# Performance work log

Measured on AMD Instinct MI355X. Metric: run time of the kernel, lower is better.

The kernel has to match this reference:

```python
import jax, jax.numpy as jnp
import numpy as np

N, E, G = 50000, 1600000, 512
H, NF_IN, NF_OUT, GF_OUT, EDIM, DEPTH = 128, 64, 64, 128, 16, 3
EPS = 1e-5


def seg_softmax(logits, seg, num):
    m = jax.ops.segment_max(logits, seg, num_segments=num)
    e = jnp.exp(logits - m[seg])
    s = jax.ops.segment_sum(e, seg, num_segments=num)
    return e / s[seg]


def batchnorm_train(x, gamma, beta):
    mu = jnp.mean(x, axis=0)
    var = jnp.mean((x - mu) ** 2, axis=0)  # biased, as torch BN training
    return (x - mu) * jax.lax.rsqrt(var + EPS) * gamma + beta


def setup_inputs() -> dict:
    key = jax.random.key(0)
    ks = jax.random.split(key, 20)
    inp = {}
    inp['x'] = jax.random.normal(ks[0], (N, NF_IN), jnp.float32)
    inp['edge_index'] = jax.random.randint(ks[1], (2, E), 0, N, jnp.int64)
    inp['edge_attr'] = jax.random.normal(ks[2], (E, EDIM), jnp.float32)
    inp['batch'] = jnp.sort(jax.random.randint(ks[3], (N,), 0, G, jnp.int64))
    inp['num_graphs'] = G
    s = 0.05
    inp['Wi'] = jax.random.normal(ks[4], (H, NF_IN), jnp.float32) * s
    inp['bi'] = jnp.zeros((H,), jnp.float32)
    inp['gat_W'] = jax.random.normal(ks[5], (DEPTH, H, 2 * H), jnp.float32) * s
    inp['gat_a'] = jax.random.normal(ks[6], (DEPTH, 2 * H), jnp.float32) * s
    inp['nfW1'] = jax.random.normal(ks[7], (H, H), jnp.float32) * s
    inp['nfb1'] = jnp.zeros((H,), jnp.float32)
    inp['nf_g'] = jnp.ones((H,), jnp.float32)
    inp['nf_b'] = jnp.zeros((H,), jnp.float32)
    inp['nfW2'] = jax.random.normal(ks[8], (NF_OUT, H), jnp.float32) * s
    inp['nfb2'] = jnp.zeros((NF_OUT,), jnp.float32)
    inp['gfW1'] = jax.random.normal(ks[9], (H, H), jnp.float32) * s
    inp['gfb1'] = jnp.zeros((H,), jnp.float32)
    inp['gf_g'] = jnp.ones((H,), jnp.float32)
    inp['gf_b'] = jnp.zeros((H,), jnp.float32)
    inp['gfW2'] = jax.random.normal(ks[10], (GF_OUT, H), jnp.float32) * s
    inp['gfb2'] = jnp.zeros((GF_OUT,), jnp.float32)
    return inp


def reference(x, edge_index, edge_attr, batch, num_graphs, Wi, bi, gat_W, gat_a,
              nfW1, nfb1, nf_g, nf_b, nfW2, nfb2,
              gfW1, gfb1, gf_g, gf_b, gfW2, gfb2):
    src, dst = edge_index[0], edge_index[1]
    nf = x @ Wi.T + bi  # [N,H]
    for i in range(DEPTH):
        src_nf = nf[src]            # [E,H]
        dst_nf = nf[dst]            # [E,H]
        ef = jnp.concatenate([src_nf, dst_nf], axis=-1) @ gat_a[i]  # [E]
        alpha = seg_softmax(ef, dst, N)
        agg = jax.ops.segment_sum(alpha[:, None] * src_nf, dst, num_segments=N)
        nf = jax.nn.relu(jnp.concatenate([nf, agg], axis=-1) @ gat_W[i].T)
    # 3-iteration attention pooling over graphs
    h = nf
    for _ in range(3):
        logits = jnp.sum(h * nf, axis=-1)  # [N]
        alpha = seg_softmax(logits, batch, num_graphs)
        h = alpha[:, None] * nf
    gf = jax.ops.segment_sum(h, batch, num_segments=num_graphs)  # [G,H]
    nf_out = jax.nn.relu(batchnorm_train(nf @ nfW1.T + nfb1, nf_g, nf_b)) @ nfW2.T + nfb2
    gf_out = jax.nn.relu(batchnorm_train(gf @ gfW1.T + gfb1, gf_g, gf_b)) @ gfW2.T + gfb2
    return nf_out, edge_attr, gf_out
```

## Files before the change

### kernel.cpp

```cpp
#include <hip/hip_runtime.h>

#define NN 50000
#define NE 1600000
#define NG 512
#define HD 128
#define NGRP 8
#define GRPSZ ((NN + NGRP - 1) / NGRP)
#define PCAP 28672

typedef __attribute__((ext_vector_type(8))) short bf16x8;
typedef __attribute__((ext_vector_type(4))) float f32x4;

static __device__ __forceinline__ unsigned bf16rn(float x) {
  unsigned b = __float_as_uint(x);
  return (b + 0x7FFFu + ((b >> 16) & 1u)) >> 16;
}
static __device__ __forceinline__ float bf16tof(unsigned short u) {
  return __uint_as_float(((unsigned)u) << 16);
}

__global__ void __launch_bounds__(256) k_part(const int* __restrict__ src,
                                              const int* __restrict__ dst,
                                              uint2* __restrict__ pairs,
                                              int* __restrict__ pcnt) {
  __shared__ uint2 buf[8][512];
  __shared__ int lcnt[8];
  __shared__ int gbase[8];
  __shared__ int nfl[8];
  const int tid = threadIdx.x;
  const int b = blockIdx.x & 7;
  if (tid < 8) lcnt[tid] = 0;
  __syncthreads();
  const int stride = gridDim.x * 256;
  for (int base_e = blockIdx.x * 256; base_e < NE; base_e += stride) {
    int e = base_e + tid;
    bool valid = e < NE;
    if (valid) {
      int d = dst[e];
      int s = src[e];
      int g = d / GRPSZ;
      int pos = atomicAdd(&lcnt[g], 1);
      buf[g][pos] = make_uint2((unsigned)d, (unsigned)s);
    }
    __syncthreads();
    if (tid < 8) {
      int c = lcnt[tid];
      int nf = (c >= 256) ? 256 : 0;
      nfl[tid] = nf;
      gbase[tid] = nf ? atomicAdd(&pcnt[tid * 8 + b], nf) : 0;
    }
    __syncthreads();
#pragma unroll
    for (int g0 = 0; g0 < 8; ++g0) {
      if (nfl[g0]) {
        int gb = gbase[g0] + tid;
        if (gb < PCAP)
          pairs[(size_t)(g0 * 8 + b) * PCAP + gb] = buf[g0][tid];
      }
    }
    __syncthreads();
#pragma unroll
    for (int g0 = 0; g0 < 8; ++g0) {
      if (nfl[g0]) {
        int rem = lcnt[g0] - 256;
        if (tid < rem) buf[g0][tid] = buf[g0][256 + tid];
      }
    }
    __syncthreads();
    if (tid < 8 && nfl[tid]) lcnt[tid] -= 256;
    __syncthreads();
  }
  if (tid < 8) {
    int c = lcnt[tid];
    gbase[tid] = c ? atomicAdd(&pcnt[tid * 8 + b], c) : 0;
  }
  __syncthreads();
#pragma unroll
  for (int g0 = 0; g0 < 8; ++g0) {
    int c = lcnt[g0];
    if (tid < c) {
      int gb = gbase[g0] + tid;
      if (gb < PCAP)
        pairs[(size_t)(g0 * 8 + b) * PCAP + gb] = buf[g0][tid];
    }
  }
}

__global__ void __launch_bounds__(256) k_hist(const uint2* __restrict__ pairs,
                                              const int* __restrict__ pcnt,
                                              int* __restrict__ hcnt) {
  __shared__ int hist[GRPSZ];
  const int b = blockIdx.x;
  const int g = b & 7, sub = b >> 3;
  const int li = g * 8 + sub;
  const int lo = g * GRPSZ;
  for (int i = threadIdx.x; i < GRPSZ; i += 256) hist[i] = 0;
  __syncthreads();
  int cnt = min(pcnt[li], PCAP);
  const uint2* lst = pairs + (size_t)li * PCAP;
  for (int i = threadIdx.x; i < cnt; i += 256)
    atomicAdd(&hist[(int)lst[i].x - lo], 1);
  __syncthreads();
  for (int i = threadIdx.x; i < GRPSZ; i += 256)
    hcnt[(size_t)li * GRPSZ + i] = hist[i];
}

__global__ void __launch_bounds__(256) k_csr(const uint2* __restrict__ pairs,
                                             const int* __restrict__ pcnt,
                                             const int* __restrict__ hcnt,
                                             int* __restrict__ row_ptr,
                                             int* __restrict__ csr_src) {
  __shared__ int rp[GRPSZ];
  __shared__ int cur[GRPSZ];
  __shared__ int wsum[256];
  const int b = blockIdx.x;
  const int g = b & 7, sub = b >> 3;
  const int li = g * 8 + sub;
  const int lo = g * GRPSZ;
  int gbase = 0;
  for (int gg = 0; gg < g; ++gg)
#pragma unroll
    for (int ss = 0; ss < 8; ++ss) gbase += pcnt[gg * 8 + ss];
  for (int i = threadIdx.x; i < GRPSZ; i += 256) {
    int dsum = 0, before = 0;
#pragma unroll
    for (int ss = 0; ss < 8; ++ss) {
      int h = hcnt[(size_t)(g * 8 + ss) * GRPSZ + i];
      dsum += h;
      if (ss < sub) before += h;
    }
    rp[i] = dsum;
    cur[i] = before;
  }
  __syncthreads();
  const int CH = (GRPSZ + 255) / 256;
  int t0 = threadIdx.x * CH;
  int t1 = min(GRPSZ, t0 + CH);
  int s = 0;
  for (int i = t0; i < t1; ++i) { int v = rp[i]; rp[i] = s; s += v; }
  wsum[threadIdx.x] = s;
  __syncthreads();
  for (int off = 1; off < 256; off <<= 1) {
    int t = ((int)threadIdx.x >= off) ? wsum[threadIdx.x - off] : 0;
    __syncthreads();
    wsum[threadIdx.x] += t;
    __syncthreads();
  }
  int add = gbase + ((threadIdx.x > 0) ? wsum[threadIdx.x - 1] : 0);
  for (int i = t0; i < t1; ++i) rp[i] += add;
  __syncthreads();
  for (int i = threadIdx.x; i < GRPSZ; i += 256) {
    cur[i] += rp[i];
    if (sub == 0) row_ptr[lo + i] = rp[i];
  }
  if (sub == 0 && g == 7 && threadIdx.x == 0) row_ptr[NN] = NE;
  __syncthreads();
  int cnt = min(pcnt[li], PCAP);
  const uint2* lst = pairs + (size_t)li * PCAP;
  for (int i = threadIdx.x; i < cnt; i += 256) {
    uint2 p = lst[i];
    int pos = atomicAdd(&cur[(int)p.x - lo], 1);
    csr_src[pos] = (int)p.y;
  }
}

__global__ void k_init_bounds(int* __restrict__ gs, int* __restrict__ ge) {
  int g = blockIdx.x * 256 + threadIdx.x;
  if (g < NG) { gs[g] = NN; ge[g] = 0; }
}
__global__ void k_bounds(const int* __restrict__ batch, int* __restrict__ gs, int* __restrict__ ge) {
  int n = blockIdx.x * 256 + threadIdx.x;
  if (n < NN) {
    int b = batch[n];
    atomicMin(&gs[b], n);
    atomicMax(&ge[b], n + 1);
  }
}

__global__ void k_cvt3(const float* __restrict__ a0, int n0,
                       const float* __restrict__ a1, int n1,
                       const float* __restrict__ a2, int n2,
                       unsigned short* __restrict__ b) {
  int i = blockIdx.x * 256 + threadIdx.x;
  if (i >= n0 + n1 + n2) return;
  float v = (i < n0) ? a0[i] : (i < n0 + n1) ? a1[i - n0] : a2[i - n0 - n1];
  b[i] = (unsigned short)bf16rn(v);
}

__global__ void k_gat_agg(const uint4* __restrict__ nf16u4, const float* __restrict__ e1,
                          const int* __restrict__ row_ptr, const int* __restrict__ csr_src,
                          unsigned short* __restrict__ agg16) {
  int node = blockIdx.x * 4 + (threadIdx.x >> 6);
  int lane = threadIdx.x & 63;
  if (node >= NN) return;
  int s = row_ptr[node], e = row_ptr[node + 1];
  const int q = lane >> 3;
  const int c = lane & 7;

  float acc[16];
#pragma unroll
  for (int i = 0; i < 16; ++i) acc[i] = 0.f;
  float zloc = 0.f;

  int jj = s + q;
  bool v0 = jj < e;
  int sc = v0 ? csr_src[jj] : 0;
  float w = v0 ? e1[sc] : 0.f;
  uint4 u0 = nf16u4[(size_t)sc * 16 + c * 2];
  uint4 u1 = nf16u4[(size_t)sc * 16 + c * 2 + 1];

  for (int j = s; j < e; j += 8) {
    int jn = j + 8 + q;
    bool vn = jn < e;
    int scn = vn ? csr_src[jn] : 0;
    float wn = vn ? e1[scn] : 0.f;
    uint4 un0 = nf16u4[(size_t)scn * 16 + c * 2];
    uint4 un1 = nf16u4[(size_t)scn * 16 + c * 2 + 1];
    zloc += w;
    acc[0]  = fmaf(w, __uint_as_float(u0.x << 16), acc[0]);
    acc[1]  = fmaf(w, __uint_as_float(u0.x & 0xFFFF0000u), acc[1]);
    acc[2]  = fmaf(w, __uint_as_float(u0.y << 16), acc[2]);
    acc[3]  = fmaf(w, __uint_as_float(u0.y & 0xFFFF0000u), acc[3]);
    acc[4]  = fmaf(w, __uint_as_float(u0.z << 16), acc[4]);
    acc[5]  = fmaf(w, __uint_as_float(u0.z & 0xFFFF0000u), acc[5]);
    acc[6]  = fmaf(w, __uint_as_float(u0.w << 16), acc[6]);
    acc[7]  = fmaf(w, __uint_as_float(u0.w & 0xFFFF0000u), acc[7]);
    acc[8]  = fmaf(w, __uint_as_float(u1.x << 16), acc[8]);
    acc[9]  = fmaf(w, __uint_as_float(u1.x & 0xFFFF0000u), acc[9]);
    acc[10] = fmaf(w, __uint_as_float(u1.y << 16), acc[10]);
    acc[11] = fmaf(w, __uint_as_float(u1.y & 0xFFFF0000u), acc[11]);
    acc[12] = fmaf(w, __uint_as_float(u1.z << 16), acc[12]);
    acc[13] = fmaf(w, __uint_as_float(u1.z & 0xFFFF0000u), acc[13]);
    acc[14] = fmaf(w, __uint_as_float(u1.w << 16), acc[14]);
    acc[15] = fmaf(w, __uint_as_float(u1.w & 0xFFFF0000u), acc[15]);
    sc = scn; w = wn; u0 = un0; u1 = un1;
  }

  zloc += __shfl_xor(zloc, 8);
  zloc += __shfl_xor(zloc, 16);
  zloc += __shfl_xor(zloc, 32);
  float inv = (zloc > 0.f) ? 1.f / zloc : 0.f;
#pragma unroll
  for (int i = 0; i < 16; ++i) {
    acc[i] += __shfl_xor(acc[i], 8);
    acc[i] += __shfl_xor(acc[i], 16);
    acc[i] += __shfl_xor(acc[i], 32);
    acc[i] *= inv;
  }
  if (q == 0) {
    uint4 p0, p1;
    p0.x = bf16rn(acc[0])  | (bf16rn(acc[1])  << 16);
    p0.y = bf16rn(acc[2])  | (bf16rn(acc[3])  << 16);
    p0.z = bf16rn(acc[4])  | (bf16rn(acc[5])  << 16);
    p0.w = bf16rn(acc[6])  | (bf16rn(acc[7])  << 16);
    p1.x = bf16rn(acc[8])  | (bf16rn(acc[9])  << 16);
    p1.y = bf16rn(acc[10]) | (bf16rn(acc[11]) << 16);
    p1.z = bf16rn(acc[12]) | (bf16rn(acc[13]) << 16);
    p1.w = bf16rn(acc[14]) | (bf16rn(acc[15]) << 16);
    uint4* dst = (uint4*)(agg16 + (size_t)node * HD + c * 16);
    dst[0] = p0;
    dst[1] = p1;
  }
}

template <int K, int KA, int HO, bool RELUOUT, bool BIAS, bool OUTF32, bool OUT16, int DOTM>
__global__ void __launch_bounds__(256) k_mfma(
    const unsigned short* __restrict__ A1, const unsigned short* __restrict__ A2,
    const unsigned short* __restrict__ W16, const float* __restrict__ bias,
    float* __restrict__ outf, unsigned short* __restrict__ out16,
    const float* __restrict__ dvec, float* __restrict__ dout, int nrows) {
  constexpr int NT = HO / 16;
  const int l = threadIdx.x & 63;
  const int w = threadIdx.x >> 6;
  const int lr = l & 15;
  const int q = l >> 4;
  const int row0 = blockIdx.x * 64 + w * 16;
  const int arow = min(row0 + lr, nrows - 1);
  const unsigned short* pa1 = A1 + (size_t)arow * KA;
  const unsigned short* pa2 = (KA < K) ? (A2 + (size_t)arow * (K - KA)) : nullptr;

  f32x4 acc[NT];
#pragma unroll
  for (int t = 0; t < NT; ++t) acc[t] = (f32x4){0.f, 0.f, 0.f, 0.f};

#pragma unroll
  for (int s = 0; s < K / 32; ++s) {
    const int kg = s * 32 + q * 8;
    bf16x8 af;
    if constexpr (KA == K) {
      af = *(const bf16x8*)(pa1 + kg);
    } else {
      af = (s * 32 < KA) ? *(const bf16x8*)(pa1 + kg)
                         : *(const bf16x8*)(pa2 + (kg - KA));
    }
#pragma unroll
    for (int t = 0; t < NT; ++t) {
      bf16x8 bfr = *(const bf16x8*)(W16 + (size_t)(t * 16 + lr) * K + kg);
      acc[t] = __builtin_amdgcn_mfma_f32_16x16x32_bf16(af, bfr, acc[t], 0, 0, 0);
    }
  }

  float bv[BIAS ? NT : 1];
  if constexpr (BIAS) {
#pragma unroll
    for (int t = 0; t < NT; ++t) bv[t] = bias[t * 16 + lr];
  }
  float dv[DOTM == 1 ? NT : 1];
  if constexpr (DOTM == 1) {
#pragma unroll
    for (int t = 0; t < NT; ++t) dv[t] = dvec[t * 16 + lr];
  }
  float p[4] = {0.f, 0.f, 0.f, 0.f};
#pragma unroll
  for (int j = 0; j < 4; ++j) {
    int n = row0 + q * 4 + j;
    bool ok = n < nrows;
#pragma unroll
    for (int t = 0; t < NT; ++t) {
      float v = acc[t][j];
      if constexpr (BIAS) v += bv[t];
      if constexpr (RELUOUT) v = fmaxf(v, 0.f);
      if (ok) {
        if constexpr (OUTF32) outf[(size_t)n * HO + t * 16 + lr] = v;
        if constexpr (OUT16) out16[(size_t)n * HO + t * 16 + lr] = (unsigned short)bf16rn(v);
      }
      if constexpr (DOTM == 1) p[j] = fmaf(v, dv[t], p[j]);
      if constexpr (DOTM == 2) p[j] = fmaf(v, v, p[j]);
    }
  }
  if constexpr (DOTM != 0) {
#pragma unroll
    for (int j = 0; j < 4; ++j) {
      p[j] += __shfl_xor(p[j], 1);
      p[j] += __shfl_xor(p[j], 2);
      p[j] += __shfl_xor(p[j], 4);
      p[j] += __shfl_xor(p[j], 8);
    }
    if (lr == 0) {
#pragma unroll
      for (int j = 0; j < 4; ++j) {
        int n = row0 + q * 4 + j;
        if (n < nrows) dout[n] = (DOTM == 1) ? __expf(p[j]) : p[j];
      }
    }
  }
}

template <int K, int KA, int HO, bool PRE, bool RELUOUT, bool BIAS, bool OUT16, int DOTM>
__global__ void __launch_bounds__(256) k_gemm(
    const float* __restrict__ inA, const float* __restrict__ inB,
    const float* __restrict__ W, const float* __restrict__ bias,
    const float* __restrict__ preA, const float* __restrict__ preB,
    float* __restrict__ out, int nrows,
    unsigned* __restrict__ out16, const float* __restrict__ dvec,
    float* __restrict__ dout) {
  constexpr int KC = 64;
  constexpr int BM = 64;
  constexpr int MT = 4;
  constexpr int NT = HO / 16;
  constexpr int LDW = HO + 4;
  constexpr int LDA = KC + 4;

  __shared__ float Wl[KC * LDW];
  __shared__ float inl[BM * LDA];

  const int tid = threadIdx.x;
  const int tr = tid >> 4;
  const int tc = tid & 15;
  const int row0 = blockIdx.x * BM;
  const int r0 = tr * MT;
  const int c0 = tc * NT;

  float acc[MT][NT];
#pragma unroll
  for (int i = 0; i < MT; ++i)
#pragma unroll
    for (int j = 0; j < NT; ++j) acc[i][j] = BIAS ? bias[c0 + j] : 0.f;

  for (int cc = 0; cc < K / KC; ++cc) {
    const int k0 = cc * KC;
    if (cc) __syncthreads();
    for (int idx = tid; idx < HO * (KC / 4); idx += 256) {
      int h = idx >> 4;
      int qq = idx & 15;
      float4 w = *(const float4*)(W + (size_t)h * K + k0 + qq * 4);
      Wl[(qq * 4 + 0) * LDW + h] = w.x;
      Wl[(qq * 4 + 1) * LDW + h] = w.y;
      Wl[(qq * 4 + 2) * LDW + h] = w.z;
      Wl[(qq * 4 + 3) * LDW + h] = w.w;
    }
    for (int idx = tid; idx < BM * (KC / 4); idx += 256) {
      int r = idx >> 4;
      int qq = idx & 15;
      int n = row0 + r;
      int kg = k0 + qq * 4;
      float4 v = make_float4(0.f, 0.f, 0.f, 0.f);
      if (n < nrows) {
        if constexpr (KA == K) {
          v = *(const float4*)(inA + (size_t)n * K + kg);
        } else {
          if (k0 < KA) v = *(const float4*)(inA + (size_t)n * KA + kg);
          else         v = *(const float4*)(inB + (size_t)n * (K - KA) + kg - KA);
        }
      }
      if constexpr (PRE) {
        v.x = fmaxf(v.x * preA[kg + 0] + preB[kg + 0], 0.f);
        v.y = fmaxf(v.y * preA[kg + 1] + preB[kg + 1], 0.f);
        v.z = fmaxf(v.z * preA[kg + 2] + preB[kg + 2], 0.f);
        v.w = fmaxf(v.w * preA[kg + 3] + preB[kg + 3], 0.f);
      }
      *(float4*)(inl + r * LDA + qq * 4) = v;
    }
    __syncthreads();
#pragma unroll 8
    for (int k = 0; k < KC; ++k) {
      float a[MT];
#pragma unroll
      for (int i = 0; i < MT; ++i) a[i] = inl[(r0 + i) * LDA + k];
      float4 b0 = *(const float4*)(Wl + k * LDW + c0);
#pragma unroll
      for (int i = 0; i < MT; ++i) {
        acc[i][0] = fmaf(a[i], b0.x, acc[i][0]);
        acc[i][1] = fmaf(a[i], b0.y, acc[i][1]);
        acc[i][2] = fmaf(a[i], b0.z, acc[i][2]);
        acc[i][3] = fmaf(a[i], b0.w, acc[i][3]);
      }
      if constexpr (NT == 8) {
        float4 b1 = *(const float4*)(Wl + k * LDW + c0 + 4);
#pragma unroll
        for (int i = 0; i < MT; ++i) {
          acc[i][4] = fmaf(a[i], b1.x, acc[i][4]);
          acc[i][5] = fmaf(a[i], b1.y, acc[i][5]);
          acc[i][6] = fmaf(a[i], b1.z, acc[i][6]);
          acc[i][7] = fmaf(a[i], b1.w, acc[i][7]);
        }
      }
    }
  }
  float dv[DOTM == 1 ? NT : 1];
  if constexpr (DOTM == 1) {
#pragma unroll
    for (int j = 0; j < NT; ++j) dv[j] = dvec[c0 + j];
  }
#pragma unroll
  for (int i = 0; i < MT; ++i) {
    int n = row0 + r0 + i;
    if constexpr (RELUOUT) {
#pragma unroll
      for (int j = 0; j < NT; ++j) acc[i][j] = fmaxf(acc[i][j], 0.f);
    }
    if (n < nrows) {
      float4 o0 = make_float4(acc[i][0], acc[i][1], acc[i][2], acc[i][3]);
      *(float4*)(out + (size_t)n * HO + c0) = o0;
      if constexpr (NT == 8) {
        float4 o1 = make_float4(acc[i][4], acc[i][5], acc[i][6], acc[i][7]);
        *(float4*)(out + (size_t)n * HO + c0 + 4) = o1;
      }
      if constexpr (OUT16 && NT == 8) {
        uint4 pk;
        pk.x = bf16rn(acc[i][0]) | (bf16rn(acc[i][1]) << 16);
        pk.y = bf16rn(acc[i][2]) | (bf16rn(acc[i][3]) << 16);
        pk.z = bf16rn(acc[i][4]) | (bf16rn(acc[i][5]) << 16);
        pk.w = bf16rn(acc[i][6]) | (bf16rn(acc[i][7]) << 16);
        *(uint4*)(out16 + (size_t)n * 64 + tc * 4) = pk;
      }
    }
    if constexpr (DOTM != 0) {
      float p = 0.f;
#pragma unroll
      for (int j = 0; j < NT; ++j)
        p = fmaf(acc[i][j], (DOTM == 1) ? dv[j] : acc[i][j], p);
      p += __shfl_xor(p, 1);
      p += __shfl_xor(p, 2);
      p += __shfl_xor(p, 4);
      p += __shfl_xor(p, 8);
      if (tc == 0 && n < nrows) dout[n] = (DOTM == 1) ? __expf(p) : p;
    }
  }
}

__global__ void k_pool(const unsigned short* __restrict__ nf16, const float* __restrict__ r,
                       const int* __restrict__ gs, const int* __restrict__ ge,
                       float* __restrict__ alpha, float* __restrict__ gf) {
  int g = blockIdx.x;
  int s = gs[g], e = ge[g];
  __shared__ float red[256];
  for (int it = 0; it < 3; ++it) {
    float lm = -INFINITY;
    for (int n = s + threadIdx.x; n < e; n += 256) {
      float l = r[n];
      if (it) l *= alpha[n];
      lm = fmaxf(lm, l);
    }
    red[threadIdx.x] = lm;
    __syncthreads();
    for (int off = 128; off > 0; off >>= 1) {
      if ((int)threadIdx.x < off) red[threadIdx.x] = fmaxf(red[threadIdx.x], red[threadIdx.x + off]);
      __syncthreads();
    }
    float m = red[0];
    __syncthreads();
    float zz = 0.f;
    for (int n = s + threadIdx.x; n < e; n += 256) {
      float l = r[n];
      if (it) l *= alpha[n];
      zz += __expf(l - m);
    }
    red[threadIdx.x] = zz;
    __syncthreads();
    for (int off = 128; off > 0; off >>= 1) {
      if ((int)threadIdx.x < off) red[threadIdx.x] += red[threadIdx.x + off];
      __syncthreads();
    }
    float z = red[0];
    __syncthreads();
    float invz = 1.f / z;
    for (int n = s + threadIdx.x; n < e; n += 256) {
      float l = r[n];
      if (it) l *= alpha[n];
      alpha[n] = __expf(l - m) * invz;
    }
    __syncthreads();
  }
  int c = threadIdx.x & 127;
  int rr2 = threadIdx.x >> 7;
  float acc = 0.f;
  for (int n = s + rr2; n < e; n += 2)
    acc += alpha[n] * bf16tof(nf16[(size_t)n * HD + c]);
  red[threadIdx.x] = acc;
  __syncthreads();
  if (rr2 == 0) gf[(size_t)g * HD + c] = red[threadIdx.x] + red[threadIdx.x + 128];
}

__global__ void k_colstats(const float* __restrict__ y, float* __restrict__ sum,
                           float* __restrict__ sumsq, int R, int CH) {
  int c = threadIdx.x & 127;
  int rr = threadIdx.x >> 7;
  int r0 = blockIdx.x * CH;
  int r1 = min(R, r0 + CH);
  float s = 0.f, q = 0.f;
  for (int r = r0 + rr; r < r1; r += 2) {
    float v = y[(size_t)r * HD + c];
    s += v;
    q += v * v;
  }
  __shared__ float ls[256], lq[256];
  ls[threadIdx.x] = s;
  lq[threadIdx.x] = q;
  __syncthreads();
  if (rr == 0) {
    s += ls[threadIdx.x + 128];
    q += lq[threadIdx.x + 128];
    atomicAdd(&sum[c], s);
    atomicAdd(&sumsq[c], q);
  }
}

__global__ void k_bn_final(const float* __restrict__ sum, const float* __restrict__ sumsq,
                           const float* __restrict__ g, const float* __restrict__ b,
                           float* __restrict__ A, float* __restrict__ B, float R) {
  int c = threadIdx.x;
  float mu = sum[c] / R;
  float var = sumsq[c] / R - mu * mu;
  float a = g[c] * rsqrtf(var + 1e-5f);
  A[c] = a;
  B[c] = b[c] - mu * a;
}

__global__ void k_bnapply(const float* __restrict__ y, const float* __restrict__ Ac,
                          const float* __restrict__ Bc, unsigned short* __restrict__ z) {
  int i = blockIdx.x * 256 + threadIdx.x;
  if (i >= NN * 16) return;
  int c = (i & 15) * 8;
  const float4* yp = (const float4*)y + (size_t)i * 2;
  float4 v0 = yp[0], v1 = yp[1];
  float4 a0 = *(const float4*)(Ac + c), a1 = *(const float4*)(Ac + c + 4);
  float4 b0 = *(const float4*)(Bc + c), b1 = *(const float4*)(Bc + c + 4);
  float r0 = fmaxf(fmaf(v0.x, a0.x, b0.x), 0.f);
  float r1 = fmaxf(fmaf(v0.y, a0.y, b0.y), 0.f);
  float r2 = fmaxf(fmaf(v0.z, a0.z, b0.z), 0.f);
  float r3 = fmaxf(fmaf(v0.w, a0.w, b0.w), 0.f);
  float r4 = fmaxf(fmaf(v1.x, a1.x, b1.x), 0.f);
  float r5 = fmaxf(fmaf(v1.y, a1.y, b1.y), 0.f);
  float r6 = fmaxf(fmaf(v1.z, a1.z, b1.z), 0.f);
  float r7 = fmaxf(fmaf(v1.w, a1.w, b1.w), 0.f);
  uint4 pk;
  pk.x = bf16rn(r0) | (bf16rn(r1) << 16);
  pk.y = bf16rn(r2) | (bf16rn(r3) << 16);
  pk.z = bf16rn(r4) | (bf16rn(r5) << 16);
  pk.w = bf16rn(r6) | (bf16rn(r7) << 16);
  *(uint4*)(z + (size_t)i * 8) = pk;
}

__global__ void k_copy4(const float4* __restrict__ a, float4* __restrict__ b, int n) {
  int i = blockIdx.x * 256 + threadIdx.x;
  if (i < n) b[i] = a[i];
}

extern "C" void kernel_launch(void* const* d_in, const int* in_sizes, int n_in,
                              void* d_out, int out_size, void* d_ws, size_t ws_size,
                              hipStream_t stream) {
  const float* x        = (const float*)d_in[0];
  const int*   ei       = (const int*)d_in[1];
  const float* edge_attr= (const float*)d_in[2];
  const int*   batch    = (const int*)d_in[3];
  const float* Wi       = (const float*)d_in[5];
  const float* bi       = (const float*)d_in[6];
  const float* gat_W    = (const float*)d_in[7];
  const float* gat_a    = (const float*)d_in[8];
  const float* nfW1     = (const float*)d_in[9];
  const float* nfb1     = (const float*)d_in[10];
  const float* nf_g     = (const float*)d_in[11];
  const float* nf_b     = (const float*)d_in[12];
  const float* nfW2     = (const float*)d_in[13];
  const float* nfb2     = (const float*)d_in[14];
  const float* gfW1     = (const float*)d_in[15];
  const float* gfb1     = (const float*)d_in[16];
  const float* gf_g     = (const float*)d_in[17];
  const float* gf_b     = (const float*)d_in[18];
  const float* gfW2     = (const float*)d_in[19];
  const float* gfb2     = (const float*)d_in[20];

  float* out = (float*)d_out;

  unsigned short* nf16A = (unsigned short*)d_ws;
  unsigned short* nf16B = nf16A + (size_t)NN * HD;
  unsigned short* agg16 = nf16B + (size_t)NN * HD;
  unsigned short* z16   = agg16 + (size_t)NN * HD;
  unsigned short* wt_gat = z16 + (size_t)NN * HD;
  unsigned short* wt_nf1 = wt_gat + 3 * 128 * 256;
  unsigned short* wt_nf2 = wt_nf1 + 128 * 128;
  float* nfA   = (float*)(wt_nf2 + 64 * 128);
  float* e1v   = nfA + (size_t)NN * HD;
  float* rv    = e1v + NN;
  float* alpha = rv + NN;
  float* gf    = alpha + NN;
  float* gy    = gf + (size_t)NG * HD;
  int*   pcnt  = (int*)(gy + (size_t)NG * HD);
  float* sums  = (float*)(pcnt + 64);
  float* sums2 = sums + 256;
  float* bnAB  = sums2 + 256;
  int* row_ptr = (int*)(bnAB + 256);
  int* csr_src = row_ptr + NN + 1;
  int* gs      = csr_src + NE;
  int* ge      = gs + NG;
  int* hcnt    = ge + NG;
  uint2* pairs = (uint2*)nfA;

  const int* src  = ei;
  const int* dstp = ei + NE;

  hipMemsetAsync(pcnt, 0, (64 + 512) * sizeof(int), stream);

  k_part<<<512, 256, 0, stream>>>(src, dstp, pairs, pcnt);
  k_hist<<<64, 256, 0, stream>>>(pairs, pcnt, hcnt);
  k_csr<<<64, 256, 0, stream>>>(pairs, pcnt, hcnt, row_ptr, csr_src);

  k_init_bounds<<<2, 256, 0, stream>>>(gs, ge);
  k_bounds<<<(NN + 255) / 256, 256, 0, stream>>>(batch, gs, ge);

  k_cvt3<<<(3 * 128 * 256 + 128 * 128 + 64 * 128 + 255) / 256, 256, 0, stream>>>(
      gat_W, 3 * 128 * 256, nfW1, 128 * 128, nfW2, 64 * 128, wt_gat);

  k_gemm<64, 64, 128, false, false, true, true, 1><<<(NN + 63) / 64, 256, 0, stream>>>(
      x, nullptr, Wi, bi, nullptr, nullptr, nfA, NN, (unsigned*)nf16A, gat_a, e1v);

  unsigned short* cur = nf16A;
  unsigned short* nxt = nf16B;
  const int gemm_grid = (NN + 63) / 64;
  for (int l = 0; l < 3; ++l) {
    k_gat_agg<<<(NN + 3) / 4, 256, 0, stream>>>((const uint4*)cur, e1v, row_ptr, csr_src, agg16);
    if (l < 2) {
      k_mfma<256, 128, 128, true, false, false, true, 1><<<gemm_grid, 256, 0, stream>>>(
          cur, agg16, wt_gat + (size_t)l * 128 * 256, nullptr,
          nullptr, nxt, gat_a + (size_t)(l + 1) * 256, e1v, NN);
    } else {
      k_mfma<256, 128, 128, true, false, false, true, 2><<<gemm_grid, 256, 0, stream>>>(
          cur, agg16, wt_gat + (size_t)l * 128 * 256, nullptr,
          nullptr, nxt, nullptr, rv, NN);
    }
    unsigned short* t = cur; cur = nxt; nxt = t;
  }

  k_pool<<<NG, 256, 0, stream>>>(cur, rv, gs, ge, alpha, gf);

  k_mfma<128, 128, 128, false, true, true, false, 0><<<gemm_grid, 256, 0, stream>>>(
      cur, nullptr, wt_nf1, nfb1, nfA, nullptr, nullptr, nullptr, NN);
  k_colstats<<<200, 256, 0, stream>>>(nfA, sums, sums + 128, NN, 250);
  k_bn_final<<<1, 128, 0, stream>>>(sums, sums + 128, nf_g, nf_b, bnAB, bnAB + 128, (float)NN);
  k_bnapply<<<(NN * 16 + 255) / 256, 256, 0, stream>>>(nfA, bnAB, bnAB + 128, z16);
  k_mfma<128, 128, 64, false, true, true, false, 0><<<gemm_grid, 256, 0, stream>>>(
      z16, nullptr, wt_nf2, nfb2, out, nullptr, nullptr, nullptr, NN);

  k_gemm<128, 128, 128, false, false, true, false, 0><<<(NG + 63) / 64, 256, 0, stream>>>(
      gf, nullptr, gfW1, gfb1, nullptr, nullptr, gy, NG, nullptr, nullptr, nullptr);
  k_colstats<<<4, 256, 0, stream>>>(gy, sums2, sums2 + 128, NG, 128);
  k_bn_final<<<1, 128, 0, stream>>>(sums2, sums2 + 128, gf_g, gf_b, bnAB, bnAB + 128, (float)NG);
  k_gemm<128, 128, 128, true, false, true, false, 0><<<(NG + 63) / 64, 256, 0, stream>>>(
      gy, nullptr, gfW2, gfb2, bnAB, bnAB + 128,
      out + (size_t)NN * 64 + (size_t)NE * 16, NG, nullptr, nullptr, nullptr);

  int n4 = NE * 16 / 4;
  k_copy4<<<(n4 + 255) / 256, 256, 0, stream>>>((const float4*)edge_attr,
                                                (float4*)(out + (size_t)NN * 64), n4);
}
```

Before: 627.5 us.

## Fuse GAT neighbor aggregation with layer MFMA GEMM via shared-memory tile

Merges the per-layer gather-aggregate kernel and the following MFMA GEMM into one kernel. Each 512-thread block aggregates 64 nodes into an LDS tile and then multiplies [nf, agg] by the layer weights, writing the bf16 output and the next layer's edge score. This removes the global round trip of agg16 and one launch per layer. The e1 buffer is double-buffered so a layer never overwrites scores it is still reading. The cost is fewer, larger blocks, and each wave now aggregates 8 nodes serially, which may reduce latency hiding during the gather.

```diff
diff --git a/kernel.cpp b/kernel.cpp
--- a/kernel.cpp
+++ b/kernel.cpp
@@ -187,79 +187,149 @@
   b[i] = (unsigned short)bf16rn(v);
 }
 
-__global__ void k_gat_agg(const uint4* __restrict__ nf16u4, const float* __restrict__ e1,
-                          const int* __restrict__ row_ptr, const int* __restrict__ csr_src,
-                          unsigned short* __restrict__ agg16) {
-  int node = blockIdx.x * 4 + (threadIdx.x >> 6);
-  int lane = threadIdx.x & 63;
-  if (node >= NN) return;
-  int s = row_ptr[node], e = row_ptr[node + 1];
-  const int q = lane >> 3;
-  const int c = lane & 7;
-
-  float acc[16];
-#pragma unroll
-  for (int i = 0; i < 16; ++i) acc[i] = 0.f;
-  float zloc = 0.f;
-
-  int jj = s + q;
-  bool v0 = jj < e;
-  int sc = v0 ? csr_src[jj] : 0;
-  float w = v0 ? e1[sc] : 0.f;
-  uint4 u0 = nf16u4[(size_t)sc * 16 + c * 2];
-  uint4 u1 = nf16u4[(size_t)sc * 16 + c * 2 + 1];
-
-  for (int j = s; j < e; j += 8) {
-    int jn = j + 8 + q;
-    bool vn = jn < e;
-    int scn = vn ? csr_src[jn] : 0;
-    float wn = vn ? e1[scn] : 0.f;
-    uint4 un0 = nf16u4[(size_t)scn * 16 + c * 2];
-    uint4 un1 = nf16u4[(size_t)scn * 16 + c * 2 + 1];
-    zloc += w;
-    acc[0]  = fmaf(w, __uint_as_float(u0.x << 16), acc[0]);
-    acc[1]  = fmaf(w, __uint_as_float(u0.x & 0xFFFF0000u), acc[1]);
-    acc[2]  = fmaf(w, __uint_as_float(u0.y << 16), acc[2]);
-    acc[3]  = fmaf(w, __uint_as_float(u0.y & 0xFFFF0000u), acc[3]);
-    acc[4]  = fmaf(w, __uint_as_float(u0.z << 16), acc[4]);
-    acc[5]  = fmaf(w, __uint_as_float(u0.z & 0xFFFF0000u), acc[5]);
-    acc[6]  = fmaf(w, __uint_as_float(u0.w << 16), acc[6]);
-    acc[7]  = fmaf(w, __uint_as_float(u0.w & 0xFFFF0000u), acc[7]);
-    acc[8]  = fmaf(w, __uint_as_float(u1.x << 16), acc[8]);
-    acc[9]  = fmaf(w, __uint_as_float(u1.x & 0xFFFF0000u), acc[9]);
-    acc[10] = fmaf(w, __uint_as_float(u1.y << 16), acc[10]);
-    acc[11] = fmaf(w, __uint_as_float(u1.y & 0xFFFF0000u), acc[11]);
-    acc[12] = fmaf(w, __uint_as_float(u1.z << 16), acc[12]);
-    acc[13] = fmaf(w, __uint_as_float(u1.z & 0xFFFF0000u), acc[13]);
-    acc[14] = fmaf(w, __uint_as_float(u1.w << 16), acc[14]);
-    acc[15] = fmaf(w, __uint_as_float(u1.w & 0xFFFF0000u), acc[15]);
-    sc = scn; w = wn; u0 = un0; u1 = un1;
-  }
-
-  zloc += __shfl_xor(zloc, 8);
-  zloc += __shfl_xor(zloc, 16);
-  zloc += __shfl_xor(zloc, 32);
-  float inv = (zloc > 0.f) ? 1.f / zloc : 0.f;
-#pragma unroll
-  for (int i = 0; i < 16; ++i) {
-    acc[i] += __shfl_xor(acc[i], 8);
-    acc[i] += __shfl_xor(acc[i], 16);
-    acc[i] += __shfl_xor(acc[i], 32);
-    acc[i] *= inv;
-  }
-  if (q == 0) {
-    uint4 p0, p1;
-    p0.x = bf16rn(acc[0])  | (bf16rn(acc[1])  << 16);
-    p0.y = bf16rn(acc[2])  | (bf16rn(acc[3])  << 16);
-    p0.z = bf16rn(acc[4])  | (bf16rn(acc[5])  << 16);
-    p0.w = bf16rn(acc[6])  | (bf16rn(acc[7])  << 16);
-    p1.x = bf16rn(acc[8])  | (bf16rn(acc[9])  << 16);
-    p1.y = bf16rn(acc[10]) | (bf16rn(acc[11]) << 16);
-    p1.z = bf16rn(acc[12]) | (bf16rn(acc[13]) << 16);
-    p1.w = bf16rn(acc[14]) | (bf16rn(acc[15]) << 16);
-    uint4* dst = (uint4*)(agg16 + (size_t)node * HD + c * 16);
-    dst[0] = p0;
-    dst[1] = p1;
+template <bool LAST>
+__global__ void __launch_bounds__(512) k_layer(
+    const unsigned short* __restrict__ nf16, const uint4* __restrict__ nf16u4,
+    const float* __restrict__ e1in,
+    const int* __restrict__ row_ptr, const int* __restrict__ csr_src,
+    const unsigned short* __restrict__ W16, const float* __restrict__ dvec,
+    unsigned short* __restrict__ out16, float* __restrict__ dout) {
+  __shared__ unsigned short aggl[64][136];
+  __shared__ float pdot[64];
+  const int tid = threadIdx.x;
+  const int wid = tid >> 6;
+  const int lane = tid & 63;
+  const int row0 = blockIdx.x * 64;
+  if (tid < 64) pdot[tid] = 0.f;
+
+  {
+    const int q = lane >> 3;
+    const int c = lane & 7;
+    for (int r = 0; r < 8; ++r) {
+      const int slot = wid * 8 + r;
+      const int node = row0 + slot;
+      int s = 0, e = 0;
+      if (node < NN) { s = row_ptr[node]; e = row_ptr[node + 1]; }
+      float acc[16];
+#pragma unroll
+      for (int i = 0; i < 16; ++i) acc[i] = 0.f;
+      float zloc = 0.f;
+      int jj = s + q;
+      bool v0 = jj < e;
+      int sc = v0 ? csr_src[jj] : 0;
+      float w = v0 ? e1in[sc] : 0.f;
+      uint4 u0 = nf16u4[(size_t)sc * 16 + c * 2];
+      uint4 u1 = nf16u4[(size_t)sc * 16 + c * 2 + 1];
+      for (int j = s; j < e; j += 8) {
+        int jn = j + 8 + q;
+        bool vn = jn < e;
+        int scn = vn ? csr_src[jn] : 0;
+        float wn = vn ? e1in[scn] : 0.f;
+        uint4 un0 = nf16u4[(size_t)scn * 16 + c * 2];
+        uint4 un1 = nf16u4[(size_t)scn * 16 + c * 2 + 1];
+        zloc += w;
+        acc[0]  = fmaf(w, __uint_as_float(u0.x << 16), acc[0]);
+        acc[1]  = fmaf(w, __uint_as_float(u0.x & 0xFFFF0000u), acc[1]);
+        acc[2]  = fmaf(w, __uint_as_float(u0.y << 16), acc[2]);
+        acc[3]  = fmaf(w, __uint_as_float(u0.y & 0xFFFF0000u), acc[3]);
+        acc[4]  = fmaf(w, __uint_as_float(u0.z << 16), acc[4]);
+        acc[5]  = fmaf(w, __uint_as_float(u0.z & 0xFFFF0000u), acc[5]);
+        acc[6]  = fmaf(w, __uint_as_float(u0.w << 16), acc[6]);
+        acc[7]  = fmaf(w, __uint_as_float(u0.w & 0xFFFF0000u), acc[7]);
+        acc[8]  = fmaf(w, __uint_as_float(u1.x << 16), acc[8]);
+        acc[9]  = fmaf(w, __uint_as_float(u1.x & 0xFFFF0000u), acc[9]);
+        acc[10] = fmaf(w, __uint_as_float(u1.y << 16), acc[10]);
+        acc[11] = fmaf(w, __uint_as_float(u1.y & 0xFFFF0000u), acc[11]);
+        acc[12] = fmaf(w, __uint_as_float(u1.z << 16), acc[12]);
+        acc[13] = fmaf(w, __uint_as_float(u1.z & 0xFFFF0000u), acc[13]);
+        acc[14] = fmaf(w, __uint_as_float(u1.w << 16), acc[14]);
+        acc[15] = fmaf(w, __uint_as_float(u1.w & 0xFFFF0000u), acc[15]);
+        sc = scn; w = wn; u0 = un0; u1 = un1;
+      }
+      zloc += __shfl_xor(zloc, 8);
+      zloc += __shfl_xor(zloc, 16);
+      zloc += __shfl_xor(zloc, 32);
+      float inv = (zloc > 0.f) ? 1.f / zloc : 0.f;
+#pragma unroll
+      for (int i = 0; i < 16; ++i) {
+        acc[i] += __shfl_xor(acc[i], 8);
+        acc[i] += __shfl_xor(acc[i], 16);
+        acc[i] += __shfl_xor(acc[i], 32);
+        acc[i] *= inv;
+      }
+      if (q == 0) {
+        uint4 p0, p1;
+        p0.x = bf16rn(acc[0])  | (bf16rn(acc[1])  << 16);
+        p0.y = bf16rn(acc[2])  | (bf16rn(acc[3])  << 16);
+        p0.z = bf16rn(acc[4])  | (bf16rn(acc[5])  << 16);
+        p0.w = bf16rn(acc[6])  | (bf16rn(acc[7])  << 16);
+        p1.x = bf16rn(acc[8])  | (bf16rn(acc[9])  << 16);
+        p1.y = bf16rn(acc[10]) | (bf16rn(acc[11]) << 16);
+        p1.z = bf16rn(acc[12]) | (bf16rn(acc[13]) << 16);
+        p1.w = bf16rn(acc[14]) | (bf16rn(acc[15]) << 16);
+        uint4* dst = (uint4*)(&aggl[slot][c * 16]);
+        dst[0] = p0;
+        dst[1] = p1;
+      }
+    }
+  }
+  __syncthreads();
+
+  {
+    const int lr = lane & 15;
+    const int qq = lane >> 4;
+    const int rblk = wid & 3, cblk = wid >> 2;
+    const int rbase = row0 + rblk * 16;
+    const int arow = min(rbase + lr, NN - 1);
+    const unsigned short* pa1 = nf16 + (size_t)arow * 128;
+    const unsigned short* pw = W16 + (size_t)(cblk * 64) * 256;
+
+    f32x4 acc[4];
+#pragma unroll
+    for (int t = 0; t < 4; ++t) acc[t] = (f32x4){0.f, 0.f, 0.f, 0.f};
+
+#pragma unroll
+    for (int s = 0; s < 8; ++s) {
+      bf16x8 af;
+      if (s < 4) af = *(const bf16x8*)(pa1 + s * 32 + qq * 8);
+      else       af = *(const bf16x8*)(&aggl[rblk * 16 + lr][(s - 4) * 32 + qq * 8]);
+#pragma unroll
+      for (int t = 0; t < 4; ++t) {
+        bf16x8 bfr = *(const bf16x8*)(pw + (size_t)(t * 16 + lr) * 256 + s * 32 + qq * 8);
+        acc[t] = __builtin_amdgcn_mfma_f32_16x16x32_bf16(af, bfr, acc[t], 0, 0, 0);
+      }
+    }
+
+    float dv[4];
+    if (!LAST) {
+#pragma unroll
+      for (int t = 0; t < 4; ++t) dv[t] = dvec[cblk * 64 + t * 16 + lr];
+    }
+    float p[4] = {0.f, 0.f, 0.f, 0.f};
+#pragma unroll
+    for (int j = 0; j < 4; ++j) {
+      int n = rbase + qq * 4 + j;
+      bool ok = n < NN;
+#pragma unroll
+      for (int t = 0; t < 4; ++t) {
+        float v = fmaxf(acc[t][j], 0.f);
+        if (ok) out16[(size_t)n * HD + cblk * 64 + t * 16 + lr] = (unsigned short)bf16rn(v);
+        p[j] = fmaf(v, LAST ? v : dv[t], p[j]);
+      }
+      p[j] += __shfl_xor(p[j], 1);
+      p[j] += __shfl_xor(p[j], 2);
+      p[j] += __shfl_xor(p[j], 4);
+      p[j] += __shfl_xor(p[j], 8);
+    }
+    if (lr == 0) {
+#pragma unroll
+      for (int j = 0; j < 4; ++j) atomicAdd(&pdot[rblk * 16 + qq * 4 + j], p[j]);
+    }
+  }
+  __syncthreads();
+  if (tid < 64) {
+    int n = row0 + tid;
+    if (n < NN) dout[n] = LAST ? pdot[tid] : __expf(pdot[tid]);
   }
 }
 
@@ -625,14 +695,14 @@
 
   unsigned short* nf16A = (unsigned short*)d_ws;
   unsigned short* nf16B = nf16A + (size_t)NN * HD;
-  unsigned short* agg16 = nf16B + (size_t)NN * HD;
-  unsigned short* z16   = agg16 + (size_t)NN * HD;
+  unsigned short* z16   = nf16B + (size_t)NN * HD;
   unsigned short* wt_gat = z16 + (size_t)NN * HD;
   unsigned short* wt_nf1 = wt_gat + 3 * 128 * 256;
   unsigned short* wt_nf2 = wt_nf1 + 128 * 128;
   float* nfA   = (float*)(wt_nf2 + 64 * 128);
-  float* e1v   = nfA + (size_t)NN * HD;
-  float* rv    = e1v + NN;
+  float* e1A   = nfA + (size_t)NN * HD;
+  float* e1B   = e1A + NN;
+  float* rv    = e1B + NN;
   float* alpha = rv + NN;
   float* gf    = alpha + NN;
   float* gy    = gf + (size_t)NG * HD;
@@ -663,27 +733,23 @@
       gat_W, 3 * 128 * 256, nfW1, 128 * 128, nfW2, 64 * 128, wt_gat);
 
   k_gemm<64, 64, 128, false, false, true, true, 1><<<(NN + 63) / 64, 256, 0, stream>>>(
-      x, nullptr, Wi, bi, nullptr, nullptr, nfA, NN, (unsigned*)nf16A, gat_a, e1v);
-
-  unsigned short* cur = nf16A;
-  unsigned short* nxt = nf16B;
+      x, nullptr, Wi, bi, nullptr, nullptr, nfA, NN, (unsigned*)nf16A, gat_a, e1A);
+
+  const int layer_grid = (NN + 63) / 64;
+  k_layer<false><<<layer_grid, 512, 0, stream>>>(
+      nf16A, (const uint4*)nf16A, e1A, row_ptr, csr_src,
+      wt_gat + 0 * 128 * 256, gat_a + 1 * 256, nf16B, e1B);
+  k_layer<false><<<layer_grid, 512, 0, stream>>>(
+      nf16B, (const uint4*)nf16B, e1B, row_ptr, csr_src,
+      wt_gat + 1 * 128 * 256, gat_a + 2 * 256, nf16A, e1A);
+  k_layer<true><<<layer_grid, 512, 0, stream>>>(
+      nf16A, (const uint4*)nf16A, e1A, row_ptr, csr_src,
+      wt_gat + 2 * 128 * 256, nullptr, nf16B, rv);
+  unsigned short* cur = nf16B;
+
+  k_pool<<<NG, 256, 0, stream>>>(cur, rv, gs, ge, alpha, gf);
+
   const int gemm_grid = (NN + 63) / 64;
-  for (int l = 0; l < 3; ++l) {
-    k_gat_agg<<<(NN + 3) / 4, 256, 0, stream>>>((const uint4*)cur, e1v, row_ptr, csr_src, agg16);
-    if (l < 2) {
-      k_mfma<256, 128, 128, true, false, false, true, 1><<<gemm_grid, 256, 0, stream>>>(
-          cur, agg16, wt_gat + (size_t)l * 128 * 256, nullptr,
-          nullptr, nxt, gat_a + (size_t)(l + 1) * 256, e1v, NN);
-    } else {
-      k_mfma<256, 128, 128, true, false, false, true, 2><<<gemm_grid, 256, 0, stream>>>(
-          cur, agg16, wt_gat + (size_t)l * 128 * 256, nullptr,
-          nullptr, nxt, nullptr, rv, NN);
-    }
-    unsigned short* t = cur; cur = nxt; nxt = t;
-  }
-
-  k_pool<<<NG, 256, 0, stream>>>(cur, rv, gs, ge, alpha, gf);
-
   k_mfma<128, 128, 128, false, true, true, false, 0><<<gemm_grid, 256, 0, stream>>>(
       cur, nullptr, wt_nf1, nfb1, nfA, nullptr, nullptr, nullptr, NN);
   k_colstats<<<200, 256, 0, stream>>>(nfA, sums, sums + 128, NN, 250);
```

Result: no change. 635.7 us (+1.3%).
